# Kernel tuning notes

Measured on AMD Instinct MI355X. Metric: run time of the kernel, lower is better.

The kernel has to match this reference:

```python
import jax, jax.numpy as jnp
import numpy as np

# ---- constants matching init_kwargs ----
ATOM_DIMS = np.array([119, 5, 12, 12, 10, 6, 6, 2, 2])
OFFSETS = np.concatenate([[0], np.cumsum(ATOM_DIMS)[:-1]])  # per-column offsets into concat table
HID = 256
HEADS = 8
BASES = 4
AGGS = 3  # sum, mean, max
LAYERS = 4
FH = HID // HEADS  # 32
N_GRAPHS = 2048
EPS = 1e-5


def setup_inputs() -> dict:
    key = jax.random.key(0)
    ks = iter(jax.random.split(key, 64))
    N, E = 50000, 800000
    x = jax.random.randint(next(ks), (N, 9), 0, 2, dtype=jnp.int64) if jax.config.jax_enable_x64 else jax.random.randint(next(ks), (N, 9), 0, 2, dtype=jnp.int32)
    edge_index = jax.random.randint(next(ks), (2, E), 0, N, dtype=x.dtype)
    batch = jnp.sort(jax.random.randint(next(ks), (N,), 0, N_GRAPHS, dtype=x.dtype))
    s = 0.05
    atom_emb = jax.random.normal(next(ks), (int(ATOM_DIMS.sum()), HID), jnp.float32) * s
    bases_W = jax.random.normal(next(ks), (LAYERS, HID, BASES * FH), jnp.float32) * s
    comb_W = jax.random.normal(next(ks), (LAYERS, HID, HEADS * BASES * AGGS), jnp.float32) * s
    comb_b = jnp.zeros((LAYERS, HEADS * BASES * AGGS), jnp.float32)
    conv_bias = jnp.zeros((LAYERS, HID), jnp.float32)
    bn_gamma = jnp.ones((LAYERS, HID), jnp.float32)
    bn_beta = jnp.zeros((LAYERS, HID), jnp.float32)
    w1 = jax.random.normal(next(ks), (HID, HID // 2), jnp.float32) * s
    g1 = jnp.ones((HID // 2,), jnp.float32)
    b1 = jnp.zeros((HID // 2,), jnp.float32)
    w2 = jax.random.normal(next(ks), (HID // 2, HID // 4), jnp.float32) * s
    g2 = jnp.ones((HID // 4,), jnp.float32)
    b2 = jnp.zeros((HID // 4,), jnp.float32)
    w3 = jax.random.normal(next(ks), (HID // 4, 1), jnp.float32) * s
    b3 = jnp.zeros((1,), jnp.float32)
    return dict(atom_emb=atom_emb, bases_W=bases_W, comb_W=comb_W, comb_b=comb_b,
                conv_bias=conv_bias, bn_gamma=bn_gamma, bn_beta=bn_beta,
                w1=w1, g1=g1, b1=b1, w2=w2, g2=g2, b2=b2, w3=w3, b3=b3,
                x=x, edge_index=edge_index, batch=batch)


def _bn(h, gamma, beta):
    mu = h.mean(0)
    var = h.var(0)
    return (h - mu) * jax.lax.rsqrt(var + EPS) * gamma + beta


def reference(atom_emb, bases_W, comb_W, comb_b, conv_bias, bn_gamma, bn_beta,
              w1, g1, b1, w2, g2, b2, w3, b3, x, edge_index, batch):
    N = x.shape[0]
    offs = jnp.asarray(OFFSETS, dtype=x.dtype)
    # AtomEncoder: sum of per-column embeddings (concat table + offsets)
    h = atom_emb[x + offs[None, :]].sum(axis=1)  # [N, HID]

    # edges with self-loops (EGConv add_self_loops=True); adj_t transposed: row=dst
    loop = jnp.arange(N, dtype=edge_index.dtype)
    dst = jnp.concatenate([edge_index[0], loop])
    src = jnp.concatenate([edge_index[1], loop])
    deg = jax.ops.segment_sum(jnp.ones_like(dst, jnp.float32), dst, num_segments=N)  # >=1

    for l in range(LAYERS):
        bases = h @ bases_W[l]                      # [N, B*FH]
        wts = (h @ comb_W[l] + comb_b[l]).reshape(N, HEADS, AGGS * BASES)
        msgs = bases[src]                            # [E+N, B*FH]
        agg_sum = jax.ops.segment_sum(msgs, dst, num_segments=N)
        agg_mean = agg_sum / deg[:, None]
        agg_max = jax.ops.segment_max(msgs, dst, num_segments=N)
        agg = jnp.stack([agg_sum, agg_mean, agg_max], axis=1)  # [N, A, B*FH]
        agg = agg.reshape(N, AGGS * BASES, FH)
        out = jnp.einsum('nhk,nkd->nhd', wts, agg).reshape(N, HID) + conv_bias[l]
        out = jax.nn.relu(_bn(out, bn_gamma[l], bn_beta[l]))
        h = h + out

    # global mean pool
    gsum = jax.ops.segment_sum(h, batch, num_segments=N_GRAPHS)
    gcnt = jax.ops.segment_sum(jnp.ones((N,), jnp.float32), batch, num_segments=N_GRAPHS)
    g = gsum / jnp.maximum(gcnt, 1.0)[:, None]

    z = jax.nn.relu(_bn(g @ w1, g1, b1))
    z = jax.nn.relu(_bn(z @ w2, g2, b2))
    return z @ w3 + b3
```

## Files before the change

### kernel.cpp

```cpp
#include <hip/hip_runtime.h>
#include <hip/hip_bf16.h>

#define HID 256
#define NGRAPH 2048

typedef __attribute__((ext_vector_type(8))) short s16x8;
typedef __attribute__((ext_vector_type(4))) float f32x4v;

__device__ inline short f2b(float f) {
    __hip_bfloat16 b = __float2bfloat16(f);
    return *reinterpret_cast<short*>(&b);
}
__device__ inline float b2f(short s) {
    return __uint_as_float(((unsigned)(unsigned short)s) << 16);
}
__device__ inline float b2f_lo(unsigned int v) {
    return __uint_as_float(v << 16);
}
__device__ inline float b2f_hi(unsigned int v) {
    return __uint_as_float(v & 0xffff0000u);
}

__global__ __launch_bounds__(256) void atom_enc(const int* __restrict__ x,
                                                const float* __restrict__ emb,
                                                short* __restrict__ hb, int N) {
    int n = blockIdx.x;
    int c = threadIdx.x;
    if (n >= N) return;
    const int offs[9] = {0, 119, 124, 136, 148, 158, 164, 170, 172};
    float s = 0.f;
#pragma unroll
    for (int j = 0; j < 9; ++j) {
        int row = x[n * 9 + j] + offs[j];
        s += emb[row * 256 + c];
    }
    hb[n * 256 + c] = f2b(s);
}

__global__ void prep_wt(const float* __restrict__ bases_W, const float* __restrict__ comb_W,
                        short* __restrict__ WT) {
    int l = blockIdx.x / 224;
    int n = blockIdx.x % 224;
    int k = threadIdx.x;
    float v = (n < 128) ? bases_W[((size_t)l * 256 + k) * 128 + n]
                        : comb_W[((size_t)l * 256 + k) * 96 + (n - 128)];
    WT[((size_t)l * 224 + n) * 256 + k] = f2b(v);
}

__global__ void init_cnt(int* cnt, int N) {
    int i = blockIdx.x * blockDim.x + threadIdx.x;
    if (i < N) cnt[i] = 1;
}

__global__ void csr_count(const int* __restrict__ ei, int E, int* cnt) {
    int e = blockIdx.x * blockDim.x + threadIdx.x;
    if (e >= E) return;
    atomicAdd(&cnt[ei[e]], 1);
}

__global__ __launch_bounds__(256) void scan_s1(const int* __restrict__ cnt, int* __restrict__ blksum, int N) {
    __shared__ int red[256];
    int base = blockIdx.x * 1024;
    int s = 0;
#pragma unroll
    for (int q = 0; q < 4; ++q) {
        int i = base + threadIdx.x * 4 + q;
        s += (i < N) ? cnt[i] : 0;
    }
    red[threadIdx.x] = s;
    __syncthreads();
    for (int off = 128; off > 0; off >>= 1) {
        if (threadIdx.x < off) red[threadIdx.x] += red[threadIdx.x + off];
        __syncthreads();
    }
    if (threadIdx.x == 0) blksum[blockIdx.x] = red[0];
}

__global__ __launch_bounds__(256) void scan_s2(int* __restrict__ blksum, int nb, int* __restrict__ row_ptr, int N) {
    __shared__ int buf[256];
    int v = (threadIdx.x < nb) ? blksum[threadIdx.x] : 0;
    buf[threadIdx.x] = v;
    __syncthreads();
    for (int off = 1; off < 256; off <<= 1) {
        int t = (threadIdx.x >= off) ? buf[threadIdx.x - off] : 0;
        __syncthreads();
        buf[threadIdx.x] += t;
        __syncthreads();
    }
    if (threadIdx.x < nb) blksum[threadIdx.x] = buf[threadIdx.x] - v;
    if (threadIdx.x == 0) row_ptr[N] = buf[255];
}

__global__ __launch_bounds__(256) void scan_s3(const int* __restrict__ cnt, const int* __restrict__ blksum,
                                               int* __restrict__ row_ptr, int* __restrict__ woff, int N) {
    __shared__ int buf[256];
    int base = blockIdx.x * 1024;
    int i0 = base + threadIdx.x * 4;
    int v[4];
    int s = 0;
#pragma unroll
    for (int q = 0; q < 4; ++q) {
        int i = i0 + q;
        v[q] = (i < N) ? cnt[i] : 0;
        s += v[q];
    }
    buf[threadIdx.x] = s;
    __syncthreads();
    for (int off = 1; off < 256; off <<= 1) {
        int t = (threadIdx.x >= off) ? buf[threadIdx.x - off] : 0;
        __syncthreads();
        buf[threadIdx.x] += t;
        __syncthreads();
    }
    int excl = buf[threadIdx.x] - s + blksum[blockIdx.x];
#pragma unroll
    for (int q = 0; q < 4; ++q) {
        int i = i0 + q;
        if (i < N) { row_ptr[i] = excl; woff[i] = excl; }
        excl += v[q];
    }
}

__global__ __launch_bounds__(256) void ph_hist(const int* __restrict__ ei, int E, int T,
                                               int PB, int NBK, int* __restrict__ mcnt) {
    __shared__ int hist[256];
    hist[threadIdx.x] = 0;
    __syncthreads();
    int base = blockIdx.x * 4096;
#pragma unroll
    for (int q = 0; q < 16; ++q) {
        int i = base + q * 256 + threadIdx.x;
        if (i < T) {
            int d = (i < E) ? ei[i] : (i - E);
            atomicAdd(&hist[d >> 8], 1);
        }
    }
    __syncthreads();
    if (threadIdx.x < NBK) mcnt[threadIdx.x * PB + blockIdx.x] = hist[threadIdx.x];
}

__global__ __launch_bounds__(256) void ph_scatter(const int* __restrict__ ei, int E, int T,
                                                  int PB, int NBK, const int* __restrict__ moff,
                                                  uint2* __restrict__ pairs) {
    __shared__ int off[256];
    if (threadIdx.x < NBK) off[threadIdx.x] = moff[threadIdx.x * PB + blockIdx.x];
    __syncthreads();
    int base = blockIdx.x * 4096;
#pragma unroll
    for (int q = 0; q < 16; ++q) {
        int i = base + q * 256 + threadIdx.x;
        if (i < T) {
            int d, s;
            if (i < E) { d = ei[i]; s = ei[E + i]; }
            else       { d = i - E; s = i - E; }
            int pos = atomicAdd(&off[d >> 8], 1);
            pairs[pos] = make_uint2((unsigned)d, (unsigned)s);
        }
    }
}

__global__ __launch_bounds__(256) void ph_sort(const uint2* __restrict__ pairs,
                                               const int* __restrict__ row_ptr,
                                               const int* __restrict__ moff,
                                               int NBK, int PB, int T,
                                               int* __restrict__ srcs) {
    __shared__ int wcnt[256];
    wcnt[threadIdx.x] = 0;
    __syncthreads();
    int bin = blockIdx.x;
    int p0 = moff[bin * PB];
    int p1 = (bin + 1 < NBK) ? moff[(bin + 1) * PB] : T;
    for (int i = p0 + threadIdx.x; i < p1; i += 256) {
        uint2 u = pairs[i];
        int d = (int)u.x;
        int rank = atomicAdd(&wcnt[d & 255], 1);
        srcs[row_ptr[d] + rank] = (int)u.y;
    }
}

__global__ __launch_bounds__(256) void gemm_mfma(short* hb,
                                                 const short* __restrict__ outb,
                                                 const float* __restrict__ ss,
                                                 int do_bn,
                                                 const short* __restrict__ WT,
                                                 const float* __restrict__ cb,
                                                 short* __restrict__ bases,
                                                 float* __restrict__ wts, int N) {
    __shared__ short bs[2][32 * 256];
    int tid = threadIdx.x;
    int wid = tid >> 6;
    int lane = tid & 63;
    int m0 = blockIdx.x * 64 + wid * 16;
    int row_orig = m0 + (lane & 15);
    bool owner = (row_orig < N);
    int row_a = owner ? row_orig : (N - 1);
    int kgrp = (lane >> 4) * 8;

    s16x8 a[8];
    if (do_bn) {
#pragma unroll
        for (int i = 0; i < 8; ++i) {
            int cbase = i * 32 + kgrp;
            size_t base = (size_t)row_a * 256 + cbase;
            s16x8 hv = *(const s16x8*)&hb[base];
            s16x8 ov = *(const s16x8*)&outb[base];
            s16x8 t;
#pragma unroll
            for (int k = 0; k < 8; ++k) {
                float hf = b2f(hv[k]);
                float of = b2f(ov[k]);
                float sc = ss[cbase + k];
                float sh = ss[256 + cbase + k];
                hf += fmaxf(of * sc + sh, 0.f);
                t[k] = f2b(hf);
            }
            if (owner) *(s16x8*)&hb[base] = t;
            a[i] = t;
        }
    } else {
#pragma unroll
        for (int i = 0; i < 8; ++i) {
            size_t base = (size_t)row_a * 256 + i * 32 + kgrp;
            a[i] = *(const s16x8*)&hb[base];
        }
    }

    int st_col = tid >> 3;
    int st_kk = (tid & 7) * 32;
    int st_sw = (st_col & 7) << 4;
    int st_base = st_col * 512 + st_kk * 2;

    auto stage = [&](int buf, int t) {
        const s16x8* src = (const s16x8*)&WT[(size_t)(t * 32 + st_col) * 256 + st_kk];
        char* dst = (char*)bs[buf];
#pragma unroll
        for (int q = 0; q < 4; ++q)
            *(s16x8*)(dst + ((st_base + q * 16) ^ st_sw)) = src[q];
    };

    stage(0, 0);

    int col = lane & 15;
    int rd_base = col * 512 + (lane >> 4) * 16;
    int rd_sw = (col & 7) << 4;
    int rbase = m0 + (lane >> 4) * 4;

    for (int t = 0; t < 7; ++t) {
        __syncthreads();
        if (t + 1 < 7) stage((t + 1) & 1, t + 1);

        const char* base = (const char*)bs[t & 1];
        f32x4v c0 = {0.f, 0.f, 0.f, 0.f};
        f32x4v c1 = {0.f, 0.f, 0.f, 0.f};
#pragma unroll
        for (int i = 0; i < 8; ++i) {
            s16x8 b0 = *(const s16x8*)(base + ((rd_base + i * 64) ^ rd_sw));
            s16x8 b1 = *(const s16x8*)(base + ((rd_base + 8192 + i * 64) ^ rd_sw));
            c0 = __builtin_amdgcn_mfma_f32_16x16x32_bf16(a[i], b0, c0, 0, 0, 0);
            c1 = __builtin_amdgcn_mfma_f32_16x16x32_bf16(a[i], b1, c1, 0, 0, 0);
        }

        int cc0 = t * 32 + col;
        int cc1 = cc0 + 16;
        float cb0 = (cc0 >= 128) ? cb[cc0 - 128] : 0.f;
        float cb1 = (cc1 >= 128) ? cb[cc1 - 128] : 0.f;
#pragma unroll
        for (int r = 0; r < 4; ++r) {
            int row = rbase + r;
            if (row >= N) continue;
            float v0 = c0[r], v1 = c1[r];
            if (cc0 < 128) bases[(size_t)row * 128 + cc0] = f2b(v0);
            else wts[(size_t)row * 96 + (cc0 - 128)] = v0 + cb0;
            if (cc1 < 128) bases[(size_t)row * 128 + cc1] = f2b(v1);
            else wts[(size_t)row * 96 + (cc1 - 128)] = v1 + cb1;
        }
    }
}

__global__ __launch_bounds__(256) void agg_einsum(const short* __restrict__ bases,
                                                  const float* __restrict__ wts,
                                                  const int* __restrict__ row_ptr,
                                                  const int* __restrict__ srcs,
                                                  const float* __restrict__ cbias,
                                                  short* __restrict__ outp,
                                                  float* __restrict__ partial, int N) {
    __shared__ float agg_lds[4][3][128];
    __shared__ float wts_lds[4][96];
    __shared__ float red[4][256];
    int wid = threadIdx.x >> 6;
    int lane = threadIdx.x & 63;
    int n = blockIdx.x * 4 + wid;
    bool valid = (n < N);

    int r0 = 0, r1 = 0;
    if (valid) {
        r0 = row_ptr[n];
        r1 = row_ptr[n + 1];
        wts_lds[wid][lane] = wts[(size_t)n * 96 + lane];
        if (lane < 32) wts_lds[wid][64 + lane] = wts[(size_t)n * 96 + 64 + lane];
    }

    int g = lane & 31;
    int half = lane >> 5;
    const short* bp = bases + 4 * g;
    const float NI = -3.402823466e+38f;
    float sA0 = 0.f, sA1 = 0.f, sA2 = 0.f, sA3 = 0.f;
    float sB0 = 0.f, sB1 = 0.f, sB2 = 0.f, sB3 = 0.f;
    float mA0 = NI, mA1 = NI, mA2 = NI, mA3 = NI;
    float mB0 = NI, mB1 = NI, mB2 = NI, mB3 = NI;

#define GACC8(S, s0_, s1_, s2_, s3_, m0_, m1_, m2_, m3_)                     \
    {                                                                        \
        uint2 v = *(const uint2*)&bp[(size_t)(S) * 128];                     \
        float f0 = b2f_lo(v.x), f1 = b2f_hi(v.x);                            \
        float f2 = b2f_lo(v.y), f3 = b2f_hi(v.y);                            \
        s0_ += f0; s1_ += f1; s2_ += f2; s3_ += f3;                          \
        m0_ = fmaxf(m0_, f0); m1_ = fmaxf(m1_, f1);                          \
        m2_ = fmaxf(m2_, f2); m3_ = fmaxf(m3_, f3);                          \
    }

    int r = r0;
    while (r < r1) {
        int chunk = r1 - r;
        if (chunk > 64) chunk = 64;
        int sidx = (lane < chunk) ? srcs[r + lane] : 0;
        int npair = chunk >> 1;
        int jp = 0;
        for (; jp + 4 <= npair; jp += 4) {
            int e0 = (jp + 0) * 2 + half, e1 = (jp + 1) * 2 + half;
            int e2 = (jp + 2) * 2 + half, e3 = (jp + 3) * 2 + half;
            int s0 = __shfl(sidx, e0), s1 = __shfl(sidx, e1);
            int s2 = __shfl(sidx, e2), s3 = __shfl(sidx, e3);
            GACC8(s0, sA0, sA1, sA2, sA3, mA0, mA1, mA2, mA3);
            GACC8(s1, sB0, sB1, sB2, sB3, mB0, mB1, mB2, mB3);
            GACC8(s2, sA0, sA1, sA2, sA3, mA0, mA1, mA2, mA3);
            GACC8(s3, sB0, sB1, sB2, sB3, mB0, mB1, mB2, mB3);
        }
        for (; jp < npair; ++jp) {
            int e0 = jp * 2 + half;
            int s0 = __shfl(sidx, e0);
            GACC8(s0, sA0, sA1, sA2, sA3, mA0, mA1, mA2, mA3);
        }
        if (chunk & 1) {
            int s0 = __shfl(sidx, chunk - 1);
            if (half == 0) {
                GACC8(s0, sB0, sB1, sB2, sB3, mB0, mB1, mB2, mB3);
            }
        }
        r += chunk;
    }
#undef GACC8

    float accs[4] = {0.f, 0.f, 0.f, 0.f};
    if (valid) {
        float s0 = sA0 + sB0, s1 = sA1 + sB1, s2 = sA2 + sB2, s3 = sA3 + sB3;
        float m0 = fmaxf(mA0, mB0), m1 = fmaxf(mA1, mB1);
        float m2 = fmaxf(mA2, mB2), m3 = fmaxf(mA3, mB3);
        s0 += __shfl_xor(s0, 32); s1 += __shfl_xor(s1, 32);
        s2 += __shfl_xor(s2, 32); s3 += __shfl_xor(s3, 32);
        m0 = fmaxf(m0, __shfl_xor(m0, 32)); m1 = fmaxf(m1, __shfl_xor(m1, 32));
        m2 = fmaxf(m2, __shfl_xor(m2, 32)); m3 = fmaxf(m3, __shfl_xor(m3, 32));

        float inv = 1.0f / (float)(r1 - r0);
        if (half == 0) {
            float4 sv = make_float4(s0, s1, s2, s3);
            float4 mv = make_float4(s0 * inv, s1 * inv, s2 * inv, s3 * inv);
            float4 xv = make_float4(m0, m1, m2, m3);
            *(float4*)&agg_lds[wid][0][4 * g] = sv;
            *(float4*)&agg_lds[wid][1][4 * g] = mv;
            *(float4*)&agg_lds[wid][2][4 * g] = xv;
        }

        asm volatile("s_waitcnt lgkmcnt(0)" ::: "memory");

#pragma unroll
        for (int j = 0; j < 4; ++j) {
            int o = lane + 64 * j;
            int hh = o >> 5;
            int d = o & 31;
            float acc = cbias[o];
#pragma unroll
            for (int k = 0; k < 12; ++k)
                acc = fmaf(wts_lds[wid][hh * 12 + k], agg_lds[wid][k >> 2][(k & 3) * 32 + d], acc);
            outp[(size_t)n * 256 + o] = f2b(acc);
            accs[j] = acc;
        }
    }
#pragma unroll
    for (int j = 0; j < 4; ++j) red[wid][lane + 64 * j] = accs[j];
    __syncthreads();
    int c = threadIdx.x;
    float s = (red[0][c] + red[1][c]) + (red[2][c] + red[3][c]);
    float s2 = (red[0][c] * red[0][c] + red[1][c] * red[1][c]) +
               (red[2][c] * red[2][c] + red[3][c] * red[3][c]);
    partial[((size_t)blockIdx.x * 2 + 0) * 256 + c] = s;
    partial[((size_t)blockIdx.x * 2 + 1) * 256 + c] = s2;
}

__global__ __launch_bounds__(256) void bn_reduce(const float* __restrict__ partial, int NB,
                                                 float* __restrict__ partial2) {
    int t = threadIdx.x;
    int chunk = (NB + 255) / 256;
    int rbeg = blockIdx.x * chunk;
    int rend = min(NB, rbeg + chunk);
    float s = 0.f, s2 = 0.f;
    for (int r = rbeg; r < rend; ++r) {
        s += partial[((size_t)r * 2 + 0) * 256 + t];
        s2 += partial[((size_t)r * 2 + 1) * 256 + t];
    }
    partial2[((size_t)blockIdx.x * 2 + 0) * 256 + t] = s;
    partial2[((size_t)blockIdx.x * 2 + 1) * 256 + t] = s2;
}

__global__ void bn_stats(const float* __restrict__ v, int N, int C, float* __restrict__ partial) {
    int c = threadIdx.x;
    float s = 0.f, s2 = 0.f;
    for (int r = blockIdx.x; r < N; r += gridDim.x) {
        float t = v[r * C + c];
        s += t; s2 += t * t;
    }
    partial[(blockIdx.x * 2 + 0) * C + c] = s;
    partial[(blockIdx.x * 2 + 1) * C + c] = s2;
}

__global__ __launch_bounds__(256) void bn_finalize(const float* __restrict__ partial, int NB, int C, int N,
                                                   const float* __restrict__ gamma, const float* __restrict__ beta,
                                                   float* __restrict__ ss) {
    int c = blockIdx.x;
    float s = 0.f, s2 = 0.f;
    for (int b = threadIdx.x; b < NB; b += 256) {
        s += partial[((size_t)b * 2 + 0) * C + c];
        s2 += partial[((size_t)b * 2 + 1) * C + c];
    }
#pragma unroll
    for (int off = 32; off > 0; off >>= 1) {
        s += __shfl_down(s, off);
        s2 += __shfl_down(s2, off);
    }
    __shared__ float wsum[4][2];
    int wid = threadIdx.x >> 6;
    int lane = threadIdx.x & 63;
    if (lane == 0) { wsum[wid][0] = s; wsum[wid][1] = s2; }
    __syncthreads();
    if (threadIdx.x == 0) {
        s = (wsum[0][0] + wsum[1][0]) + (wsum[2][0] + wsum[3][0]);
        s2 = (wsum[0][1] + wsum[1][1]) + (wsum[2][1] + wsum[3][1]);
        float invN = 1.0f / (float)N;
        float mu = s * invN;
        float var = fmaxf(s2 * invN - mu * mu, 0.f);
        float sc = gamma[c] * rsqrtf(var + 1e-5f);
        ss[c] = sc;
        ss[C + c] = beta[c] - mu * sc;
    }
}

__global__ void bn_apply_res8(short* __restrict__ hb, const short* __restrict__ outp,
                              const float* __restrict__ ss, int total8) {
    int i = blockIdx.x * blockDim.x + threadIdx.x;
    if (i >= total8) return;
    int c0 = (i * 8) & 255;
    size_t base = (size_t)i * 8;
    s16x8 hv = *(const s16x8*)&hb[base];
    s16x8 ov = *(const s16x8*)&outp[base];
    s16x8 t;
#pragma unroll
    for (int k = 0; k < 8; ++k) {
        float hf = b2f(hv[k]);
        float of = b2f(ov[k]);
        hf += fmaxf(of * ss[c0 + k] + ss[256 + c0 + k], 0.f);
        t[k] = f2b(hf);
    }
    *(s16x8*)&hb[base] = t;
}

__global__ void bn_apply(float* __restrict__ z, const float* __restrict__ ss, int total, int C, int Cmask) {
    int i = blockIdx.x * blockDim.x + threadIdx.x;
    if (i >= total) return;
    int c = i & Cmask;
    z[i] = fmaxf(z[i] * ss[c] + ss[C + c], 0.f);
}

__device__ int lower_bound_dev(const int* a, int n, int v) {
    int lo = 0, hi = n;
    while (lo < hi) {
        int mid = (lo + hi) >> 1;
        if (a[mid] < v) lo = mid + 1; else hi = mid;
    }
    return lo;
}

__global__ __launch_bounds__(256) void pool_kernel(const short* __restrict__ hb,
                                                   const int* __restrict__ batch, int N,
                                                   float* __restrict__ g) {
    __shared__ int sh[2];
    if (threadIdx.x == 0) {
        sh[0] = lower_bound_dev(batch, N, (int)blockIdx.x);
        sh[1] = lower_bound_dev(batch, N, (int)blockIdx.x + 1);
    }
    __syncthreads();
    int s0 = sh[0], s1 = sh[1];
    float s = 0.f;
    for (int r = s0; r < s1; ++r) s += b2f(hb[(size_t)r * 256 + threadIdx.x]);
    float cnt = (float)(s1 - s0);
    g[blockIdx.x * 256 + threadIdx.x] = s / fmaxf(cnt, 1.0f);
}

__global__ void mlp_gemm(const float* __restrict__ in, const float* __restrict__ W,
                         float* __restrict__ outp, int K, int C) {
    extern __shared__ float srow[];
    int r = blockIdx.x;
    for (int k = threadIdx.x; k < K; k += blockDim.x) srow[k] = in[r * K + k];
    __syncthreads();
    int c = threadIdx.x;
    float acc = 0.f;
    for (int k = 0; k < K; ++k) acc = fmaf(srow[k], W[k * C + c], acc);
    outp[r * C + c] = acc;
}

__global__ void final_gemm(const float* __restrict__ z2, const float* __restrict__ w3,
                           const float* __restrict__ b3, float* __restrict__ outp, int G) {
    int g = blockIdx.x * blockDim.x + threadIdx.x;
    if (g >= G) return;
    float acc = b3[0];
    for (int k = 0; k < 64; ++k) acc = fmaf(z2[g * 64 + k], w3[k], acc);
    outp[g] = acc;
}

extern "C" void kernel_launch(void* const* d_in, const int* in_sizes, int n_in,
                              void* d_out, int out_size, void* d_ws, size_t ws_size,
                              hipStream_t stream) {
    const float* atom_emb = (const float*)d_in[0];
    const float* bases_W = (const float*)d_in[1];
    const float* comb_W = (const float*)d_in[2];
    const float* comb_b = (const float*)d_in[3];
    const float* conv_bias = (const float*)d_in[4];
    const float* bn_gamma = (const float*)d_in[5];
    const float* bn_beta = (const float*)d_in[6];
    const float* w1 = (const float*)d_in[7];
    const float* g1 = (const float*)d_in[8];
    const float* b1 = (const float*)d_in[9];
    const float* w2 = (const float*)d_in[10];
    const float* g2 = (const float*)d_in[11];
    const float* b2 = (const float*)d_in[12];
    const float* w3 = (const float*)d_in[13];
    const float* b3 = (const float*)d_in[14];
    const int* x = (const int*)d_in[15];
    const int* edge_index = (const int*)d_in[16];
    const int* batch = (const int*)d_in[17];
    float* out = (float*)d_out;

    const int N = in_sizes[15] / 9;
    const int E = in_sizes[16] / 2;
    const int G = NGRAPH;
    const int T = E + N;
    const int NCHUNK = (N + 1023) / 1024;
    const int PB = (T + 4095) / 4096;
    const int NBK = (N + 255) >> 8;
    const int M = NBK * PB;
    const int MCHUNK = (M + 1023) / 1024;
    const int AGG_NB = (N + 3) / 4;

    char* p = (char*)d_ws;
    auto alloc = [&](size_t bytes) -> void* {
        void* r = (void*)p;
        p += (bytes + 255) & ~(size_t)255;
        return r;
    };
    short* hb = (short*)alloc((size_t)N * 256 * 2);
    short* outb = (short*)alloc((size_t)N * 256 * 2);
    short* bases = (short*)alloc((size_t)N * 128 * 2);
    float* wts = (float*)alloc((size_t)N * 96 * 4);
    short* WT = (short*)alloc((size_t)4 * 224 * 256 * 2);
    int* row_ptr = (int*)alloc((size_t)(N + 1) * 4);
    int* cnt = (int*)alloc((size_t)N * 4);
    int* woff = (int*)alloc((size_t)N * 4);
    int* blksum = (int*)alloc((size_t)256 * 4);
    int* mcnt = (int*)alloc((size_t)(M + 1) * 4);
    int* moff = (int*)alloc((size_t)(M + 1) * 4);
    int* srcs = (int*)alloc((size_t)T * 4);
    float* partial = (float*)alloc((size_t)AGG_NB * 2 * 256 * 4);
    float* partial2 = (float*)alloc((size_t)256 * 2 * 256 * 4);
    float* ss = (float*)alloc((size_t)2 * 256 * 4);
    float* g = (float*)alloc((size_t)G * 256 * 4);
    float* z1 = (float*)alloc((size_t)G * 128 * 4);
    float* z2 = (float*)alloc((size_t)G * 64 * 4);
    uint2* pairs = (uint2*)alloc((size_t)T * 8);

    atom_enc<<<N, 256, 0, stream>>>(x, atom_emb, hb, N);
    prep_wt<<<4 * 224, 256, 0, stream>>>(bases_W, comb_W, WT);

    init_cnt<<<(N + 255) / 256, 256, 0, stream>>>(cnt, N);
    csr_count<<<(E + 255) / 256, 256, 0, stream>>>(edge_index, E, cnt);
    scan_s1<<<NCHUNK, 256, 0, stream>>>(cnt, blksum, N);
    scan_s2<<<1, 256, 0, stream>>>(blksum, NCHUNK, row_ptr, N);
    scan_s3<<<NCHUNK, 256, 0, stream>>>(cnt, blksum, row_ptr, woff, N);

    ph_hist<<<PB, 256, 0, stream>>>(edge_index, E, T, PB, NBK, mcnt);
    scan_s1<<<MCHUNK, 256, 0, stream>>>(mcnt, blksum, M);
    scan_s2<<<1, 256, 0, stream>>>(blksum, MCHUNK, moff, M);
    scan_s3<<<MCHUNK, 256, 0, stream>>>(mcnt, blksum, moff, moff, M);
    ph_scatter<<<PB, 256, 0, stream>>>(edge_index, E, T, PB, NBK, moff, pairs);
    ph_sort<<<NBK, 256, 0, stream>>>(pairs, row_ptr, moff, NBK, PB, T, srcs);

    for (int l = 0; l < 4; ++l) {
        const short* WTl = WT + (size_t)l * 224 * 256;
        const float* cb = comb_b + (size_t)l * 96;
        const float* cbias = conv_bias + (size_t)l * 256;
        const float* gam = bn_gamma + (size_t)l * 256;
        const float* bet = bn_beta + (size_t)l * 256;

        gemm_mfma<<<(N + 63) / 64, 256, 0, stream>>>(hb, outb, ss, l > 0 ? 1 : 0,
                                                     WTl, cb, bases, wts, N);
        agg_einsum<<<AGG_NB, 256, 0, stream>>>(bases, wts, row_ptr, srcs, cbias, outb, partial, N);
        bn_reduce<<<256, 256, 0, stream>>>(partial, AGG_NB, partial2);
        bn_finalize<<<256, 256, 0, stream>>>(partial2, 256, 256, N, gam, bet, ss);
    }
    {
        int total8 = N * 256 / 8;
        bn_apply_res8<<<(total8 + 255) / 256, 256, 0, stream>>>(hb, outb, ss, total8);
    }

    pool_kernel<<<G, 256, 0, stream>>>(hb, batch, N, g);

    mlp_gemm<<<G, 128, 256 * 4, stream>>>(g, w1, z1, 256, 128);
    bn_stats<<<64, 128, 0, stream>>>(z1, G, 128, partial);
    bn_finalize<<<128, 256, 0, stream>>>(partial, 64, 128, G, g1, b1, ss);
    bn_apply<<<(G * 128 + 255) / 256, 256, 0, stream>>>(z1, ss, G * 128, 128, 127);

    mlp_gemm<<<G, 64, 128 * 4, stream>>>(z1, w2, z2, 128, 64);
    bn_stats<<<64, 64, 0, stream>>>(z2, G, 64, partial);
    bn_finalize<<<64, 256, 0, stream>>>(partial, 64, 64, G, g2, b2, ss);
    bn_apply<<<(G * 64 + 255) / 256, 256, 0, stream>>>(z2, ss, G * 64, 64, 63);

    final_gemm<<<(G + 255) / 256, 256, 0, stream>>>(z2, w3, b3, out, G);
}
```

Measured before the change: 567.7 us.

## Store combine weights in bf16 and fuse final BN-apply passes into consumers

```diff
diff --git a/kernel.cpp b/kernel.cpp
--- a/kernel.cpp
+++ b/kernel.cpp
@@ -185,7 +185,7 @@
                                                  const short* __restrict__ WT,
                                                  const float* __restrict__ cb,
                                                  short* __restrict__ bases,
-                                                 float* __restrict__ wts, int N) {
+                                                 short* __restrict__ wts, int N) {
     __shared__ short bs[2][32 * 256];
     int tid = threadIdx.x;
     int wid = tid >> 6;
@@ -270,15 +270,15 @@
             if (row >= N) continue;
             float v0 = c0[r], v1 = c1[r];
             if (cc0 < 128) bases[(size_t)row * 128 + cc0] = f2b(v0);
-            else wts[(size_t)row * 96 + (cc0 - 128)] = v0 + cb0;
+            else wts[(size_t)row * 96 + (cc0 - 128)] = f2b(v0 + cb0);
             if (cc1 < 128) bases[(size_t)row * 128 + cc1] = f2b(v1);
-            else wts[(size_t)row * 96 + (cc1 - 128)] = v1 + cb1;
+            else wts[(size_t)row * 96 + (cc1 - 128)] = f2b(v1 + cb1);
         }
     }
 }
 
 __global__ __launch_bounds__(256) void agg_einsum(const short* __restrict__ bases,
-                                                  const float* __restrict__ wts,
+                                                  const short* __restrict__ wts,
                                                   const int* __restrict__ row_ptr,
                                                   const int* __restrict__ srcs,
                                                   const float* __restrict__ cbias,
@@ -296,8 +296,8 @@
     if (valid) {
         r0 = row_ptr[n];
         r1 = row_ptr[n + 1];
-        wts_lds[wid][lane] = wts[(size_t)n * 96 + lane];
-        if (lane < 32) wts_lds[wid][64 + lane] = wts[(size_t)n * 96 + 64 + lane];
+        wts_lds[wid][lane] = b2f(wts[(size_t)n * 96 + lane]);
+        if (lane < 32) wts_lds[wid][64 + lane] = b2f(wts[(size_t)n * 96 + 64 + lane]);
     }
 
     int g = lane & 31;
@@ -454,32 +454,6 @@
     }
 }
 
-__global__ void bn_apply_res8(short* __restrict__ hb, const short* __restrict__ outp,
-                              const float* __restrict__ ss, int total8) {
-    int i = blockIdx.x * blockDim.x + threadIdx.x;
-    if (i >= total8) return;
-    int c0 = (i * 8) & 255;
-    size_t base = (size_t)i * 8;
-    s16x8 hv = *(const s16x8*)&hb[base];
-    s16x8 ov = *(const s16x8*)&outp[base];
-    s16x8 t;
-#pragma unroll
-    for (int k = 0; k < 8; ++k) {
-        float hf = b2f(hv[k]);
-        float of = b2f(ov[k]);
-        hf += fmaxf(of * ss[c0 + k] + ss[256 + c0 + k], 0.f);
-        t[k] = f2b(hf);
-    }
-    *(s16x8*)&hb[base] = t;
-}
-
-__global__ void bn_apply(float* __restrict__ z, const float* __restrict__ ss, int total, int C, int Cmask) {
-    int i = blockIdx.x * blockDim.x + threadIdx.x;
-    if (i >= total) return;
-    int c = i & Cmask;
-    z[i] = fmaxf(z[i] * ss[c] + ss[C + c], 0.f);
-}
-
 __device__ int lower_bound_dev(const int* a, int n, int v) {
     int lo = 0, hi = n;
     while (lo < hi) {
@@ -490,6 +464,8 @@
 }
 
 __global__ __launch_bounds__(256) void pool_kernel(const short* __restrict__ hb,
+                                                   const short* __restrict__ outb,
+                                                   const float* __restrict__ ss,
                                                    const int* __restrict__ batch, int N,
                                                    float* __restrict__ g) {
     __shared__ int sh[2];
@@ -499,10 +475,16 @@
     }
     __syncthreads();
     int s0 = sh[0], s1 = sh[1];
+    int c = threadIdx.x;
+    float sc = ss[c], shf = ss[256 + c];
     float s = 0.f;
-    for (int r = s0; r < s1; ++r) s += b2f(hb[(size_t)r * 256 + threadIdx.x]);
+    for (int r = s0; r < s1; ++r) {
+        size_t idx = (size_t)r * 256 + c;
+        float hf = b2f(hb[idx]) + fmaxf(b2f(outb[idx]) * sc + shf, 0.f);
+        s += hf;
+    }
     float cnt = (float)(s1 - s0);
-    g[blockIdx.x * 256 + threadIdx.x] = s / fmaxf(cnt, 1.0f);
+    g[blockIdx.x * 256 + c] = s / fmaxf(cnt, 1.0f);
 }
 
 __global__ void mlp_gemm(const float* __restrict__ in, const float* __restrict__ W,
@@ -517,12 +499,30 @@
     outp[r * C + c] = acc;
 }
 
-__global__ void final_gemm(const float* __restrict__ z2, const float* __restrict__ w3,
-                           const float* __restrict__ b3, float* __restrict__ outp, int G) {
+__global__ void mlp_gemm_bn(const float* __restrict__ in, const float* __restrict__ ssb,
+                            const float* __restrict__ W,
+                            float* __restrict__ outp, int K, int C) {
+    extern __shared__ float srow[];
+    int r = blockIdx.x;
+    for (int k = threadIdx.x; k < K; k += blockDim.x)
+        srow[k] = fmaxf(in[r * K + k] * ssb[k] + ssb[K + k], 0.f);
+    __syncthreads();
+    int c = threadIdx.x;
+    float acc = 0.f;
+    for (int k = 0; k < K; ++k) acc = fmaf(srow[k], W[k * C + c], acc);
+    outp[r * C + c] = acc;
+}
+
+__global__ void final_gemm_bn(const float* __restrict__ z2, const float* __restrict__ ssb,
+                              const float* __restrict__ w3,
+                              const float* __restrict__ b3, float* __restrict__ outp, int G) {
     int g = blockIdx.x * blockDim.x + threadIdx.x;
     if (g >= G) return;
     float acc = b3[0];
-    for (int k = 0; k < 64; ++k) acc = fmaf(z2[g * 64 + k], w3[k], acc);
+    for (int k = 0; k < 64; ++k) {
+        float z = fmaxf(z2[g * 64 + k] * ssb[k] + ssb[64 + k], 0.f);
+        acc = fmaf(z, w3[k], acc);
+    }
     outp[g] = acc;
 }
 
@@ -569,7 +569,7 @@
     short* hb = (short*)alloc((size_t)N * 256 * 2);
     short* outb = (short*)alloc((size_t)N * 256 * 2);
     short* bases = (short*)alloc((size_t)N * 128 * 2);
-    float* wts = (float*)alloc((size_t)N * 96 * 4);
+    short* wts = (short*)alloc((size_t)N * 96 * 2);
     short* WT = (short*)alloc((size_t)4 * 224 * 256 * 2);
     int* row_ptr = (int*)alloc((size_t)(N + 1) * 4);
     int* cnt = (int*)alloc((size_t)N * 4);
@@ -615,22 +615,16 @@
         bn_reduce<<<256, 256, 0, stream>>>(partial, AGG_NB, partial2);
         bn_finalize<<<256, 256, 0, stream>>>(partial2, 256, 256, N, gam, bet, ss);
     }
-    {
-        int total8 = N * 256 / 8;
-        bn_apply_res8<<<(total8 + 255) / 256, 256, 0, stream>>>(hb, outb, ss, total8);
-    }
-
-    pool_kernel<<<G, 256, 0, stream>>>(hb, batch, N, g);
+
+    pool_kernel<<<G, 256, 0, stream>>>(hb, outb, ss, batch, N, g);
 
     mlp_gemm<<<G, 128, 256 * 4, stream>>>(g, w1, z1, 256, 128);
     bn_stats<<<64, 128, 0, stream>>>(z1, G, 128, partial);
     bn_finalize<<<128, 256, 0, stream>>>(partial, 64, 128, G, g1, b1, ss);
-    bn_apply<<<(G * 128 + 255) / 256, 256, 0, stream>>>(z1, ss, G * 128, 128, 127);
-
-    mlp_gemm<<<G, 64, 128 * 4, stream>>>(z1, w2, z2, 128, 64);
+
+    mlp_gemm_bn<<<G, 64, 128 * 4, stream>>>(z1, ss, w2, z2, 128, 64);
     bn_stats<<<64, 64, 0, stream>>>(z2, G, 64, partial);
     bn_finalize<<<64, 256, 0, stream>>>(partial, 64, 64, G, g2, b2, ss);
-    bn_apply<<<(G * 64 + 255) / 256, 256, 0, stream>>>(z2, ss, G * 64, 64, 63);
-
-    final_gemm<<<(G + 255) / 256, 256, 0, stream>>>(z2, w3, b3, out, G);
-}
+
+    final_gemm_bn<<<(G + 255) / 256, 256, 0, stream>>>(z2, ss, w3, b3, out, G);
+}
```

Measured after the change: 547.4 us. -3.6%, faster.
